# Optimization experiments

Measured on AMD Instinct MI355X. Metric: run time of the kernel, lower is better.

## Reference

```python
import jax, jax.numpy as jnp
import numpy as np

B, A, OBS, NACT, H, D = 8192, 8, 128, 32, 256, 64  # batch, n_agents, obs_shape, n_actions, rnn_hidden_dim, attn_dim
N = B * A


def setup_inputs() -> dict:
    key = jax.random.key(0)
    ks = jax.random.split(key, 12)
    s = 0.02
    return {
        "o": jax.random.normal(ks[0], (N, OBS), dtype=jnp.float32),
        "o_next": jax.random.normal(ks[1], (N, OBS), dtype=jnp.float32),
        "h": jax.random.normal(ks[2], (N, H), dtype=jnp.float32),
        "actions": jax.random.uniform(ks[3], (N, A, NACT), dtype=jnp.float32),
        "wq_w": jax.random.normal(ks[4], (D, 2 * OBS), dtype=jnp.float32) * s,
        "wq_b": jnp.zeros((D,), dtype=jnp.float32),
        "wk_w": jax.random.normal(ks[5], (D, NACT), dtype=jnp.float32) * s,
        "wk_b": jnp.zeros((D,), dtype=jnp.float32),
        "wv1_w": jax.random.normal(ks[6], (D, H + NACT), dtype=jnp.float32) * s,
        "wv1_b": jnp.zeros((D,), dtype=jnp.float32),
        "wv2_w": jax.random.normal(ks[7], (NACT, D), dtype=jnp.float32) * s,
        "wv2_b": jnp.zeros((NACT,), dtype=jnp.float32),
    }


def reference(o, o_next, h, actions, wq_w, wq_b, wk_w, wk_b, wv1_w, wv1_b, wv2_w, wv2_b):
    n, a, nact = actions.shape           # [N, A, n_actions]
    d = wq_w.shape[0]                    # attn_dim
    hdim = h.shape[-1]
    b = n // a
    # query: [N, D]
    query = jnp.concatenate([o, o_next], axis=-1) @ wq_w.T + wq_b
    # key: [N, A, D]
    key = (actions.reshape(-1, nact) @ wk_w.T + wk_b).reshape(n, a, d)
    # value: repeat h per attended agent -> [B*A*A, H]
    h_rep = jnp.tile(h.reshape(b, a, hdim), (1, a, 1)).reshape(-1, hdim)
    inps_v = jnp.concatenate([h_rep, actions.reshape(-1, nact)], axis=-1)
    hid = jax.nn.relu(inps_v @ wv1_w.T + wv1_b)
    value = (hid @ wv2_w.T + wv2_b).reshape(n, a, nact)
    # attention scores with self-masked diagonal
    scale = 1.0 / (float(d) ** 0.5)
    scores = jnp.einsum('nd,nad->na', query * scale, key).reshape(b, a, a)
    eye = jnp.eye(a, dtype=bool)
    scores = jnp.where(eye[None, :, :], jnp.asarray(-1e9, scores.dtype), scores)
    attn = jax.nn.softmax(scores, axis=-1).reshape(n, a, 1)
    q = jnp.sum(value * attn, axis=1)    # [N, n_actions]
    return q
```

## Files before the change

### kernel.cpp

```cpp
#include <hip/hip_runtime.h>

typedef __attribute__((ext_vector_type(8))) short bf16x8;
typedef __attribute__((ext_vector_type(4))) float f32x4;

#define MFMA(A, B, C) __builtin_amdgcn_mfma_f32_16x16x32_bf16((A), (B), (C), 0, 0, 0)

#define OFF_TB    0
#define OFF_WT_H  128
#define OFF_WT_L  16512
#define OFF_WHV_H 32896
#define OFF_WHV_L 65664
#define OFF_WA_H  98432
#define OFF_WA_L  102528

#define SM_HV   0
#define SM_AT   17408
#define SM_SS   19456
#define SM_TOT  29184

__device__ __forceinline__ unsigned short f2bf(float v) {
    unsigned u = __builtin_bit_cast(unsigned, v);
    return (unsigned short)((u + 0x7fffu + ((u >> 16) & 1u)) >> 16);
}
__device__ __forceinline__ float bf2f(unsigned short b) {
    return __builtin_bit_cast(float, ((unsigned)b) << 16);
}
__device__ __forceinline__ ushort2 splitf(float v) {
    unsigned short h = f2bf(v);
    unsigned short l = f2bf(v - bf2f(h));
    return make_ushort2(h, l);
}
__device__ __forceinline__ void split8(float4 a, float4 b, bf16x8& hi, bf16x8& lo) {
    float v[8] = {a.x, a.y, a.z, a.w, b.x, b.y, b.z, b.w};
    bf16x8 H, L;
#pragma unroll
    for (int i = 0; i < 8; ++i) {
        ushort2 s = splitf(v[i]);
        H[i] = (short)s.x;
        L[i] = (short)s.y;
    }
    hi = H; lo = L;
}

__global__ __launch_bounds__(256) void k_setup(const float* __restrict__ wq_w,
                                               const float* __restrict__ wq_b,
                                               const float* __restrict__ wk_w,
                                               const float* __restrict__ wv1,
                                               char* __restrict__ ws) {
    int gid = blockIdx.x * 256 + threadIdx.x;
    if (gid < 8192) {
        int k = gid >> 8, c = gid & 255;
        float acc = 0.f;
#pragma unroll 8
        for (int d = 0; d < 64; ++d) acc = fmaf(wk_w[d * 32 + k], wq_w[d * 256 + c], acc);
        ushort2 s = splitf(0.125f * acc);
        ((unsigned short*)(ws + OFF_WT_H))[gid] = s.x;
        ((unsigned short*)(ws + OFF_WT_L))[gid] = s.y;
    } else if (gid < 24576) {
        int i = gid - 8192;
        ushort2 s = splitf(wv1[(i >> 8) * 288 + (i & 255)]);
        ((unsigned short*)(ws + OFF_WHV_H))[i] = s.x;
        ((unsigned short*)(ws + OFF_WHV_L))[i] = s.y;
    } else if (gid < 26624) {
        int i = gid - 24576;
        ushort2 s = splitf(wv1[(i >> 5) * 288 + 256 + (i & 31)]);
        ((unsigned short*)(ws + OFF_WA_H))[i] = s.x;
        ((unsigned short*)(ws + OFF_WA_L))[i] = s.y;
    } else if (gid < 26656) {
        int k = gid - 26624;
        float b = 0.f;
#pragma unroll 8
        for (int d = 0; d < 64; ++d) b = fmaf(wk_w[d * 32 + k], wq_b[d], b);
        ((float*)(ws + OFF_TB))[k] = 0.125f * b;
    }
}

__global__ __launch_bounds__(256, 4) void fused(
    const float* __restrict__ o, const float* __restrict__ onx,
    const float* __restrict__ h, const float* __restrict__ act,
    const float* __restrict__ wv1b, const float* __restrict__ wv2,
    const float* __restrict__ wv2b, const char* __restrict__ ws,
    float* __restrict__ out)
{
    __shared__ __align__(16) char sm[SM_TOT];
    float* HV = (float*)(sm + SM_HV);
    float* AT = (float*)(sm + SM_AT);
    short* SS = (short*)(sm + SM_SS);

    const int tid  = threadIdx.x;
    const int lane = tid & 63;
    const int wid  = tid >> 6;
    const int l15  = lane & 15;
    const int quad = lane >> 4;
    const int n0   = blockIdx.x * 64;

    const f32x4 zv = {0.f, 0.f, 0.f, 0.f};
    f32x4 acc_hv[4] = {zv, zv, zv, zv};
    f32x4 acc_t[2]  = {zv, zv};

    const int myrow = n0 + wid * 16 + l15;

    float4 xa[8], xb[8];
#pragma unroll
    for (int ch = 0; ch < 8; ++ch) {
        const float* src = (ch < 4)
            ? o   + (size_t)myrow * 128 + ch * 32 + quad * 8
            : onx + (size_t)myrow * 128 + (ch - 4) * 32 + quad * 8;
        xa[ch] = ((const float4*)src)[0];
        xb[ch] = ((const float4*)src)[1];
    }
#pragma unroll
    for (int ch = 0; ch < 8; ++ch) {
        bf16x8 Bh, Bl;
        split8(xa[ch], xb[ch], Bh, Bl);
#pragma unroll
        for (int mt = 0; mt < 2; ++mt) {
            int off = ((mt * 16 + l15) * 256 + ch * 32 + quad * 8) * 2;
            bf16x8 Ah = *(const bf16x8*)(ws + OFF_WT_H + off);
            bf16x8 Al = *(const bf16x8*)(ws + OFF_WT_L + off);
            acc_t[mt] = MFMA(Ah, Bh, acc_t[mt]);
            acc_t[mt] = MFMA(Ah, Bl, acc_t[mt]);
            acc_t[mt] = MFMA(Al, Bh, acc_t[mt]);
        }
    }
#pragma unroll
    for (int ch = 0; ch < 8; ++ch) {
        const float* src = h + (size_t)myrow * 256 + ch * 32 + quad * 8;
        xa[ch] = ((const float4*)src)[0];
        xb[ch] = ((const float4*)src)[1];
    }
#pragma unroll
    for (int ch = 0; ch < 8; ++ch) {
        bf16x8 Bh, Bl;
        split8(xa[ch], xb[ch], Bh, Bl);
#pragma unroll
        for (int mt = 0; mt < 4; ++mt) {
            int off = ((mt * 16 + l15) * 256 + ch * 32 + quad * 8) * 2;
            bf16x8 Ah = *(const bf16x8*)(ws + OFF_WHV_H + off);
            bf16x8 Al = *(const bf16x8*)(ws + OFF_WHV_L + off);
            acc_hv[mt] = MFMA(Ah, Bh, acc_hv[mt]);
            acc_hv[mt] = MFMA(Ah, Bl, acc_hv[mt]);
            acc_hv[mt] = MFMA(Al, Bh, acc_hv[mt]);
        }
    }

    const float* arow = act + (size_t)myrow * 256;
    float4 av0[8], av1[8];
#pragma unroll
    for (int j = 0; j < 8; ++j) {
        av0[j] = *(const float4*)(arow + j * 32 + quad * 4);
        av1[j] = *(const float4*)(arow + j * 32 + 16 + quad * 4);
    }

    {
        int erow = wid * 16 + l15;
#pragma unroll
        for (int mt = 0; mt < 4; ++mt) {
            int d0 = mt * 16 + quad * 4;
            float4 b = *(const float4*)&wv1b[d0];
            f32x4 a = acc_hv[mt];
            *(float4*)&HV[erow * 68 + d0] =
                make_float4(a[0] + b.x, a[1] + b.y, a[2] + b.z, a[3] + b.w);
        }
    }

    {
        float t8[8];
        const float* tb = (const float*)(ws + OFF_TB);
#pragma unroll
        for (int mt = 0; mt < 2; ++mt) {
            float4 b = *(const float4*)&tb[mt * 16 + quad * 4];
            t8[mt * 4 + 0] = acc_t[mt][0] + b.x;
            t8[mt * 4 + 1] = acc_t[mt][1] + b.y;
            t8[mt * 4 + 2] = acc_t[mt][2] + b.z;
            t8[mt * 4 + 3] = acc_t[mt][3] + b.w;
        }
        float sc[8];
#pragma unroll
        for (int j = 0; j < 8; ++j) {
            float s = 0.f;
            s = fmaf(t8[0], av0[j].x, s);
            s = fmaf(t8[1], av0[j].y, s);
            s = fmaf(t8[2], av0[j].z, s);
            s = fmaf(t8[3], av0[j].w, s);
            s = fmaf(t8[4], av1[j].x, s);
            s = fmaf(t8[5], av1[j].y, s);
            s = fmaf(t8[6], av1[j].z, s);
            s = fmaf(t8[7], av1[j].w, s);
            sc[j] = s;
        }
#pragma unroll
        for (int j = 0; j < 8; ++j) {
            sc[j] += __shfl_xor(sc[j], 16);
            sc[j] += __shfl_xor(sc[j], 32);
        }
        const int diag = l15 & 7;
        float mx = -1e30f;
#pragma unroll
        for (int j = 0; j < 8; ++j) if (j != diag) mx = fmaxf(mx, sc[j]);
        float ex[8], sum = 0.f;
#pragma unroll
        for (int j = 0; j < 8; ++j) {
            ex[j] = (j == diag) ? 0.f : __expf(sc[j] - mx);
            sum += ex[j];
        }
        float inv = 1.f / sum;
        if (quad == 0) {
            int row = wid * 16 + l15;
            *(float4*)&AT[row * 8] =
                make_float4(ex[0] * inv, ex[1] * inv, ex[2] * inv, ex[3] * inv);
            *(float4*)&AT[row * 8 + 4] =
                make_float4(ex[4] * inv, ex[5] * inv, ex[6] * inv, ex[7] * inv);
        }
    }

    bf16x8 WAh[4], WAl[4];
#pragma unroll
    for (int mt = 0; mt < 4; ++mt) {
        int off = ((mt * 16 + l15) * 32 + quad * 8) * 2;
        WAh[mt] = *(const bf16x8*)(ws + OFF_WA_H + off);
        WAl[mt] = *(const bf16x8*)(ws + OFF_WA_L + off);
    }
    __syncthreads();

#pragma unroll
    for (int half = 0; half < 2; ++half) {
        float4 bv0[4], bv1[4];
        int nbs[4], js[4];
#pragma unroll
        for (int ii = 0; ii < 4; ++ii) {
            int g   = half * 2 + (ii >> 1);
            int nt  = ii & 1;
            int njr = wid * 32 + nt * 16 + l15;
            int nb  = g * 16 + (njr >> 3);
            int j   = njr & 7;
            const float* ap = act + (size_t)(n0 + nb) * 256 + j * 32 + quad * 8;
            bv0[ii] = ((const float4*)ap)[0];
            bv1[ii] = ((const float4*)ap)[1];
            nbs[ii] = nb; js[ii] = j;
        }
#pragma unroll
        for (int ii = 0; ii < 4; ++ii) {
            int nb = nbs[ii], j = js[ii];
            bf16x8 Bh, Bl;
            split8(bv0[ii], bv1[ii], Bh, Bl);
            f32x4 accB[4] = {zv, zv, zv, zv};
#pragma unroll
            for (int mt = 0; mt < 4; ++mt) {
                accB[mt] = MFMA(WAh[mt], Bh, accB[mt]);
                accB[mt] = MFMA(WAh[mt], Bl, accB[mt]);
                accB[mt] = MFMA(WAl[mt], Bh, accB[mt]);
            }
            int hrow = (nb & ~7) + j;
            float at = AT[nb * 8 + j];
#pragma unroll
            for (int mt = 0; mt < 4; ++mt) {
                int d0 = mt * 16 + quad * 4;
                float4 hv4 = *(const float4*)&HV[hrow * 68 + d0];
                float r0 = at * fmaxf(accB[mt][0] + hv4.x, 0.f);
                float r1 = at * fmaxf(accB[mt][1] + hv4.y, 0.f);
                float r2 = at * fmaxf(accB[mt][2] + hv4.z, 0.f);
                float r3 = at * fmaxf(accB[mt][3] + hv4.w, 0.f);
#pragma unroll
                for (int m = 1; m <= 4; m <<= 1) {
                    r0 += __shfl_xor(r0, m);
                    r1 += __shfl_xor(r1, m);
                    r2 += __shfl_xor(r2, m);
                    r3 += __shfl_xor(r3, m);
                }
                if (j == 0)
                    *(ushort4*)&SS[nb * 76 + d0] =
                        make_ushort4(f2bf(r0), f2bf(r1), f2bf(r2), f2bf(r3));
            }
        }
    }
    __syncthreads();

    {
        int row = wid * 16 + l15;
        float s[64];
#pragma unroll
        for (int q = 0; q < 16; ++q) {
            ushort4 u = *(const ushort4*)&SS[row * 76 + q * 4];
            s[q*4+0] = bf2f(u.x); s[q*4+1] = bf2f(u.y);
            s[q*4+2] = bf2f(u.z); s[q*4+3] = bf2f(u.w);
        }
        float qa[8];
#pragma unroll
        for (int e0 = 0; e0 < 8; ++e0) qa[e0] = wv2b[quad * 8 + e0];
#pragma unroll
        for (int d4 = 0; d4 < 16; ++d4) {
#pragma unroll
            for (int e0 = 0; e0 < 8; ++e0) {
                float4 w = *(const float4*)&wv2[(quad * 8 + e0) * 64 + d4 * 4];
                qa[e0] = fmaf(w.x, s[d4*4+0], qa[e0]);
                qa[e0] = fmaf(w.y, s[d4*4+1], qa[e0]);
                qa[e0] = fmaf(w.z, s[d4*4+2], qa[e0]);
                qa[e0] = fmaf(w.w, s[d4*4+3], qa[e0]);
            }
        }
        float* op = out + (size_t)(n0 + row) * 32 + quad * 8;
        ((float4*)op)[0] = make_float4(qa[0], qa[1], qa[2], qa[3]);
        ((float4*)op)[1] = make_float4(qa[4], qa[5], qa[6], qa[7]);
    }
}

extern "C" void kernel_launch(void* const* d_in, const int* in_sizes, int n_in,
                              void* d_out, int out_size, void* d_ws, size_t ws_size,
                              hipStream_t stream) {
    const float* o     = (const float*)d_in[0];
    const float* onx   = (const float*)d_in[1];
    const float* h     = (const float*)d_in[2];
    const float* act   = (const float*)d_in[3];
    const float* wq_w  = (const float*)d_in[4];
    const float* wq_b  = (const float*)d_in[5];
    const float* wk_w  = (const float*)d_in[6];
    const float* wv1_w = (const float*)d_in[8];
    const float* wv1_b = (const float*)d_in[9];
    const float* wv2_w = (const float*)d_in[10];
    const float* wv2_b = (const float*)d_in[11];
    float* out = (float*)d_out;
    char* ws   = (char*)d_ws;

    k_setup<<<105, 256, 0, stream>>>(wq_w, wq_b, wk_w, wv1_w, ws);
    fused<<<1024, 256, 0, stream>>>(o, onx, h, act, wv1_b, wv2_w, wv2_b, ws, out);
}
```

Before: 269.5 us.

## Use single-wave blocks, MFMA for final projection, and hardware bf16 packing

Reorganizes the fused kernel from 4-wave blocks covering 64 rows to 1-wave blocks covering 16 rows, which shrinks shared memory and removes inter-wave barrier coupling. The final wv2 projection moves from per-thread scalar FMAs to bf16 MFMA, with the weights split into hi/lo parts. The float-to-bf16 split and pack helpers now use the HIP bf16 conversion intrinsics. The trade-off is four times as many blocks and more redundant weight loads per block.

Measured after the change: 251.3 us. 6.8% less time.

```diff
diff --git a/kernel.cpp b/kernel.cpp
--- a/kernel.cpp
+++ b/kernel.cpp
@@ -1,4 +1,5 @@
 #include <hip/hip_runtime.h>
+#include <hip/hip_bf16.h>
 
 typedef __attribute__((ext_vector_type(8))) short bf16x8;
 typedef __attribute__((ext_vector_type(4))) float f32x4;
@@ -14,9 +15,9 @@
 #define OFF_WA_L  102528
 
 #define SM_HV   0
-#define SM_AT   17408
-#define SM_SS   19456
-#define SM_TOT  29184
+#define SM_AT   4352
+#define SM_SS   4864
+#define SM_TOT  7168
 
 __device__ __forceinline__ unsigned short f2bf(float v) {
     unsigned u = __builtin_bit_cast(unsigned, v);
@@ -30,16 +31,31 @@
     unsigned short l = f2bf(v - bf2f(h));
     return make_ushort2(h, l);
 }
+
+__device__ __forceinline__ unsigned as_u32(__hip_bfloat162 v) {
+    unsigned u;
+    __builtin_memcpy(&u, &v, sizeof(u));
+    return u;
+}
+
+__device__ __forceinline__ void split2(float x, float y, unsigned& h, unsigned& l) {
+    __hip_bfloat162 h2 = __float22bfloat162_rn(make_float2(x, y));
+    float2 hf = __bfloat1622float2(h2);
+    __hip_bfloat162 l2 = __float22bfloat162_rn(make_float2(x - hf.x, y - hf.y));
+    h = as_u32(h2);
+    l = as_u32(l2);
+}
 __device__ __forceinline__ void split8(float4 a, float4 b, bf16x8& hi, bf16x8& lo) {
-    float v[8] = {a.x, a.y, a.z, a.w, b.x, b.y, b.z, b.w};
-    bf16x8 H, L;
-#pragma unroll
-    for (int i = 0; i < 8; ++i) {
-        ushort2 s = splitf(v[i]);
-        H[i] = (short)s.x;
-        L[i] = (short)s.y;
-    }
-    hi = H; lo = L;
+    uint4 H, L;
+    split2(a.x, a.y, H.x, L.x);
+    split2(a.z, a.w, H.y, L.y);
+    split2(b.x, b.y, H.z, L.z);
+    split2(b.z, b.w, H.w, L.w);
+    hi = __builtin_bit_cast(bf16x8, H);
+    lo = __builtin_bit_cast(bf16x8, L);
+}
+__device__ __forceinline__ unsigned pk2(float x, float y) {
+    return as_u32(__float22bfloat162_rn(make_float2(x, y)));
 }
 
 __global__ __launch_bounds__(256) void k_setup(const float* __restrict__ wq_w,
@@ -75,7 +91,7 @@
     }
 }
 
-__global__ __launch_bounds__(256, 4) void fused(
+__global__ __launch_bounds__(64, 4) void fused(
     const float* __restrict__ o, const float* __restrict__ onx,
     const float* __restrict__ h, const float* __restrict__ act,
     const float* __restrict__ wv1b, const float* __restrict__ wv2,
@@ -85,20 +101,17 @@
     __shared__ __align__(16) char sm[SM_TOT];
     float* HV = (float*)(sm + SM_HV);
     float* AT = (float*)(sm + SM_AT);
-    short* SS = (short*)(sm + SM_SS);
-
-    const int tid  = threadIdx.x;
-    const int lane = tid & 63;
-    const int wid  = tid >> 6;
+    unsigned short* SS = (unsigned short*)(sm + SM_SS);
+
+    const int lane = threadIdx.x;
     const int l15  = lane & 15;
     const int quad = lane >> 4;
-    const int n0   = blockIdx.x * 64;
+    const int n0   = blockIdx.x * 16;
+    const int myrow = n0 + l15;
 
     const f32x4 zv = {0.f, 0.f, 0.f, 0.f};
     f32x4 acc_hv[4] = {zv, zv, zv, zv};
     f32x4 acc_t[2]  = {zv, zv};
-
-    const int myrow = n0 + wid * 16 + l15;
 
     float4 xa[8], xb[8];
 #pragma unroll
@@ -152,16 +165,13 @@
         av1[j] = *(const float4*)(arow + j * 32 + 16 + quad * 4);
     }
 
-    {
-        int erow = wid * 16 + l15;
-#pragma unroll
-        for (int mt = 0; mt < 4; ++mt) {
-            int d0 = mt * 16 + quad * 4;
-            float4 b = *(const float4*)&wv1b[d0];
-            f32x4 a = acc_hv[mt];
-            *(float4*)&HV[erow * 68 + d0] =
-                make_float4(a[0] + b.x, a[1] + b.y, a[2] + b.z, a[3] + b.w);
-        }
+#pragma unroll
+    for (int mt = 0; mt < 4; ++mt) {
+        int d0 = mt * 16 + quad * 4;
+        float4 b = *(const float4*)&wv1b[d0];
+        f32x4 a = acc_hv[mt];
+        *(float4*)&HV[l15 * 68 + d0] =
+            make_float4(a[0] + b.x, a[1] + b.y, a[2] + b.z, a[3] + b.w);
     }
 
     {
@@ -206,10 +216,9 @@
         }
         float inv = 1.f / sum;
         if (quad == 0) {
-            int row = wid * 16 + l15;
-            *(float4*)&AT[row * 8] =
+            *(float4*)&AT[l15 * 8] =
                 make_float4(ex[0] * inv, ex[1] * inv, ex[2] * inv, ex[3] * inv);
-            *(float4*)&AT[row * 8 + 4] =
+            *(float4*)&AT[l15 * 8 + 4] =
                 make_float4(ex[4] * inv, ex[5] * inv, ex[6] * inv, ex[7] * inv);
         }
     }
@@ -223,25 +232,22 @@
     }
     __syncthreads();
 
+    const int jB  = l15 & 7;
+    const int nbh = l15 >> 3;
 #pragma unroll
     for (int half = 0; half < 2; ++half) {
         float4 bv0[4], bv1[4];
-        int nbs[4], js[4];
 #pragma unroll
         for (int ii = 0; ii < 4; ++ii) {
-            int g   = half * 2 + (ii >> 1);
-            int nt  = ii & 1;
-            int njr = wid * 32 + nt * 16 + l15;
-            int nb  = g * 16 + (njr >> 3);
-            int j   = njr & 7;
-            const float* ap = act + (size_t)(n0 + nb) * 256 + j * 32 + quad * 8;
+            int nb = (half * 4 + ii) * 2 + nbh;
+            const float* ap = act + (size_t)(n0 + nb) * 256 + jB * 32 + quad * 8;
             bv0[ii] = ((const float4*)ap)[0];
             bv1[ii] = ((const float4*)ap)[1];
-            nbs[ii] = nb; js[ii] = j;
         }
 #pragma unroll
         for (int ii = 0; ii < 4; ++ii) {
-            int nb = nbs[ii], j = js[ii];
+            int nt = half * 4 + ii;
+            int nb = nt * 2 + nbh;
             bf16x8 Bh, Bl;
             split8(bv0[ii], bv1[ii], Bh, Bl);
             f32x4 accB[4] = {zv, zv, zv, zv};
@@ -251,8 +257,8 @@
                 accB[mt] = MFMA(WAh[mt], Bl, accB[mt]);
                 accB[mt] = MFMA(WAl[mt], Bh, accB[mt]);
             }
-            int hrow = (nb & ~7) + j;
-            float at = AT[nb * 8 + j];
+            int hrow = (nb & 8) + jB;
+            float at = AT[nb * 8 + jB];
 #pragma unroll
             for (int mt = 0; mt < 4; ++mt) {
                 int d0 = mt * 16 + quad * 4;
@@ -268,40 +274,42 @@
                     r2 += __shfl_xor(r2, m);
                     r3 += __shfl_xor(r3, m);
                 }
-                if (j == 0)
-                    *(ushort4*)&SS[nb * 76 + d0] =
-                        make_ushort4(f2bf(r0), f2bf(r1), f2bf(r2), f2bf(r3));
+                if (jB == 0)
+                    *(uint2*)&SS[nb * 72 + d0] = make_uint2(pk2(r0, r1), pk2(r2, r3));
             }
         }
     }
+
+    float4 wva[4], wvb[4];
+#pragma unroll
+    for (int c = 0; c < 4; ++c) {
+        const float* wp = wv2 + ((c >> 1) * 16 + l15) * 64 + (c & 1) * 32 + quad * 8;
+        wva[c] = ((const float4*)wp)[0];
+        wvb[c] = ((const float4*)wp)[1];
+    }
     __syncthreads();
 
     {
-        int row = wid * 16 + l15;
-        float s[64];
-#pragma unroll
-        for (int q = 0; q < 16; ++q) {
-            ushort4 u = *(const ushort4*)&SS[row * 76 + q * 4];
-            s[q*4+0] = bf2f(u.x); s[q*4+1] = bf2f(u.y);
-            s[q*4+2] = bf2f(u.z); s[q*4+3] = bf2f(u.w);
-        }
-        float qa[8];
-#pragma unroll
-        for (int e0 = 0; e0 < 8; ++e0) qa[e0] = wv2b[quad * 8 + e0];
-#pragma unroll
-        for (int d4 = 0; d4 < 16; ++d4) {
-#pragma unroll
-            for (int e0 = 0; e0 < 8; ++e0) {
-                float4 w = *(const float4*)&wv2[(quad * 8 + e0) * 64 + d4 * 4];
-                qa[e0] = fmaf(w.x, s[d4*4+0], qa[e0]);
-                qa[e0] = fmaf(w.y, s[d4*4+1], qa[e0]);
-                qa[e0] = fmaf(w.z, s[d4*4+2], qa[e0]);
-                qa[e0] = fmaf(w.w, s[d4*4+3], qa[e0]);
-            }
-        }
-        float* op = out + (size_t)(n0 + row) * 32 + quad * 8;
-        ((float4*)op)[0] = make_float4(qa[0], qa[1], qa[2], qa[3]);
-        ((float4*)op)[1] = make_float4(qa[4], qa[5], qa[6], qa[7]);
+        bf16x8 Sb[2];
+#pragma unroll
+        for (int kc = 0; kc < 2; ++kc)
+            Sb[kc] = *(const bf16x8*)&SS[l15 * 72 + kc * 32 + quad * 8];
+        f32x4 acc2[2] = {zv, zv};
+#pragma unroll
+        for (int c = 0; c < 4; ++c) {
+            bf16x8 Ah, Al;
+            split8(wva[c], wvb[c], Ah, Al);
+            acc2[c >> 1] = MFMA(Ah, Sb[c & 1], acc2[c >> 1]);
+            acc2[c >> 1] = MFMA(Al, Sb[c & 1], acc2[c >> 1]);
+        }
+#pragma unroll
+        for (int et = 0; et < 2; ++et) {
+            int e0 = et * 16 + quad * 4;
+            float4 b = *(const float4*)&wv2b[e0];
+            f32x4 a = acc2[et];
+            *(float4*)&out[(size_t)(n0 + l15) * 32 + e0] =
+                make_float4(a[0] + b.x, a[1] + b.y, a[2] + b.z, a[3] + b.w);
+        }
     }
 }
 
@@ -323,5 +331,5 @@
     char* ws   = (char*)d_ws;
 
     k_setup<<<105, 256, 0, stream>>>(wq_w, wq_b, wk_w, wv1_w, ws);
-    fused<<<1024, 256, 0, stream>>>(o, onx, h, act, wv1_b, wv2_w, wv2_b, ws, out);
-}
+    fused<<<4096, 64, 0, stream>>>(o, onx, h, act, wv1_b, wv2_w, wv2_b, ws, out);
+}
```
